# Kernel tuning notes

Hardware: AMD Instinct MI355X
Metric: run time of the kernel (lower is better)

## Reference

```python
import jax, jax.numpy as jnp
import numpy as np

N, E, R = 50000, 800000, 3
IN_DIM, HID, HEADS = 128, 128, 4
C = HID // HEADS  # per-head channels = 32
NEG_SLOPE = 0.2   # GATConv default LeakyReLU slope
LN_EPS = 1e-5


def setup_inputs() -> dict:
    key = jax.random.key(0)
    ks = jax.random.split(key, 8)
    x = jax.random.normal(ks[0], (N, IN_DIM), jnp.float32)
    edge_index = jax.random.randint(ks[1], (R, 2, E), 0, N, jnp.int32)
    edge_attr = jax.random.uniform(ks[2], (R, E, 1), dtype=jnp.float32)  # unused by GATConv (edge_dim=None)
    W = jax.random.normal(ks[3], (R, IN_DIM, HID), jnp.float32) / np.float32(np.sqrt(IN_DIM))
    att_src = jax.random.normal(ks[4], (R, HEADS, C), jnp.float32) / np.float32(np.sqrt(C))
    att_dst = jax.random.normal(ks[5], (R, HEADS, C), jnp.float32) / np.float32(np.sqrt(C))
    bias = jnp.zeros((R, HID), jnp.float32)
    gate = jnp.ones((R,), jnp.float32)
    ln_gamma = jnp.ones((HID,), jnp.float32)
    ln_beta = jnp.zeros((HID,), jnp.float32)
    return dict(x=x, edge_index=edge_index, edge_attr=edge_attr, W=W,
                att_src=att_src, att_dst=att_dst, bias=bias, gate=gate,
                ln_gamma=ln_gamma, ln_beta=ln_beta)


def _gat(x, W, a_src, a_dst, b, ei):
    # One GATConv (concat heads, no self loops, eval-mode so no attn dropout).
    h = (x @ W).reshape(N, HEADS, C)                      # [N,H,C]
    alpha_src = jnp.einsum('nhc,hc->nh', h, a_src)        # [N,H]
    alpha_dst = jnp.einsum('nhc,hc->nh', h, a_dst)        # [N,H]
    src, dst = ei[0], ei[1]
    e = jax.nn.leaky_relu(alpha_src[src] + alpha_dst[dst], NEG_SLOPE)  # [E,H]
    # segment-softmax over incoming edges of each dst node
    e_max = jax.ops.segment_max(e, dst, num_segments=N)   # [N,H] (-inf for isolated nodes, never indexed)
    e_exp = jnp.exp(e - e_max[dst])                       # [E,H]
    denom = jax.ops.segment_sum(e_exp, dst, num_segments=N)
    alpha = e_exp / (denom[dst] + 1e-16)                  # [E,H]
    msg = h[src] * alpha[:, :, None]                      # [E,H,C] edge gather + weight
    out = jax.ops.segment_sum(msg, dst, num_segments=N)   # [N,H,C] scatter-aggregate
    return out.reshape(N, HID) + b


def reference(x, edge_index, edge_attr, W, att_src, att_dst, bias, gate, ln_gamma, ln_beta):
    # edge_attr is accepted but unused: GATConv was built without edge_dim.
    outs = jax.vmap(_gat, in_axes=(None, 0, 0, 0, 0, 0))(x, W, att_src, att_dst, bias, edge_index)  # [R,N,HID]
    gw = jax.nn.softmax(gate)                             # gated fusion weights [R]
    h = jnp.einsum('r,rnd->nd', gw, outs)                 # [N,HID]
    h = h + x                                             # rescale = Identity (in_dim == hid)
    mu = jnp.mean(h, axis=-1, keepdims=True)
    var = jnp.var(h, axis=-1, keepdims=True)
    h = (h - mu) / jnp.sqrt(var + LN_EPS) * ln_gamma + ln_beta
    return h, gw  # dropout is identity in eval mode
```

## Files before the change

kernel.cpp:

```cpp
#include <hip/hip_runtime.h>

#define N_NODES 50000
#define E_EDGES 800000
#define R_REL 3
#define HID 128
#define HEADS 4
#define CAP 64
#define NPART 32
#define PSIZE 1563
#define CHUNKS_A 98
#define CAP_A 448

typedef __attribute__((ext_vector_type(8))) short short8;
typedef __attribute__((ext_vector_type(4))) float float4v;

__device__ __forceinline__ unsigned short f2bf(float f) {
    unsigned int u = __float_as_uint(f);
    u += 0x7fffu + ((u >> 16) & 1u);
    return (unsigned short)(u >> 16);
}
__device__ __forceinline__ float bf_lo(unsigned int u) { return __uint_as_float(u << 16); }
__device__ __forceinline__ float bf_hi(unsigned int u) { return __uint_as_float(u & 0xffff0000u); }

#define WCONV_T (R_REL * HID * HID)
#define SETUP_BLKS 193
#define FILLA_BLKS (R_REL * CHUNKS_A)
__global__ __launch_bounds__(256) void setup_fillA_kernel(const float* __restrict__ W,
                                                          const float* __restrict__ gate,
                                                          const int* __restrict__ edge_idx,
                                                          unsigned short* __restrict__ wtb,
                                                          float* __restrict__ gw_out,
                                                          unsigned* __restrict__ regions,
                                                          int* __restrict__ bc) {
    __shared__ unsigned buf[NPART * CAP_A];
    __shared__ int lcnt[NPART];
    int bid = blockIdx.x;
    if (bid < SETUP_BLKS) {
        int tid = bid * 256 + threadIdx.x;
        if (tid < WCONV_T) {
            int r = tid >> 14, rem = tid & 16383, n = rem >> 7, k = rem & 127;
            wtb[tid] = f2bf(W[r * 16384 + k * 128 + n]);
        } else if (tid == WCONV_T) {
            float g0 = gate[0], g1 = gate[1], g2 = gate[2];
            float mg = fmaxf(g0, fmaxf(g1, g2));
            float e0 = __expf(g0 - mg), e1 = __expf(g1 - mg), e2 = __expf(g2 - mg);
            float inv = 1.f / (e0 + e1 + e2);
            gw_out[0] = e0 * inv; gw_out[1] = e1 * inv; gw_out[2] = e2 * inv;
        }
        return;
    }
    int fb = bid - SETUP_BLKS;
    int r = fb / CHUNKS_A, c = fb % CHUNKS_A;
    if (threadIdx.x < NPART) lcnt[threadIdx.x] = 0;
    __syncthreads();
    const int4* s4 = (const int4*)(edge_idx + (long)r * 2 * E_EDGES);
    const int4* d4 = (const int4*)(edge_idx + (long)r * 2 * E_EDGES + E_EDGES);
    int i0 = c * 2048;
    int i1 = i0 + 2048; if (i1 > E_EDGES / 4) i1 = E_EDGES / 4;
    for (int i = i0 + threadIdx.x; i < i1; i += 256) {
        int4 sv = s4[i];
        int4 dv = d4[i];
#pragma unroll
        for (int j = 0; j < 4; ++j) {
            int dst = (j == 0) ? dv.x : (j == 1) ? dv.y : (j == 2) ? dv.z : dv.w;
            int src = (j == 0) ? sv.x : (j == 1) ? sv.y : (j == 2) ? sv.z : sv.w;
            int p = dst / PSIZE;
            int reldst = dst - p * PSIZE;
            int pos = atomicAdd(&lcnt[p], 1);
            if (pos < CAP_A) buf[p * CAP_A + pos] = ((unsigned)reldst << 16) | (unsigned)src;
        }
    }
    __syncthreads();
    long rbase = (long)(r * CHUNKS_A + c) * NPART;
#pragma unroll 4
    for (int p = 0; p < NPART; ++p) {
        int n = lcnt[p]; if (n > CAP_A) n = CAP_A;
        unsigned* dp = regions + (rbase + p) * CAP_A;
        for (int i = threadIdx.x; i < n; i += 256) dp[i] = buf[p * CAP_A + i];
    }
    if (threadIdx.x < NPART) {
        int n = lcnt[threadIdx.x]; if (n > CAP_A) n = CAP_A;
        bc[rbase + threadIdx.x] = n;
    }
}

#define FILLB_BLKS (R_REL * NPART)
#define STRIPS 3125
#define BLK_PER_REL 782
#define GEMM_BLKS (R_REL * BLK_PER_REL)
__global__ __launch_bounds__(256) void gemm_fillB_kernel(const float* __restrict__ x,
                                                         const unsigned short* __restrict__ wtb,
                                                         unsigned short* __restrict__ hb,
                                                         const float* __restrict__ att_src,
                                                         const float* __restrict__ att_dst,
                                                         float* __restrict__ asrc,
                                                         float* __restrict__ adst,
                                                         const unsigned* __restrict__ regions,
                                                         const int* __restrict__ bc,
                                                         int* __restrict__ cnt,
                                                         unsigned short* __restrict__ slots) {
    __shared__ int lc[PSIZE];
    int bid = blockIdx.x;
    if (bid < FILLB_BLKS) {
        int r = bid / NPART, p = bid % NPART;
        int base = p * PSIZE;
        int psz = N_NODES - base; if (psz > PSIZE) psz = PSIZE;
        for (int i = threadIdx.x; i < PSIZE; i += 256) lc[i] = 0;
        __syncthreads();
        for (int c = 0; c < CHUNKS_A; ++c) {
            long rb = (long)(r * CHUNKS_A + c) * NPART + p;
            int n = bc[rb];
            const unsigned* sp = regions + rb * CAP_A;
            for (int i = threadIdx.x; i < n; i += 256) {
                unsigned e = sp[i];
                int reldst = e >> 16;
                int src = e & 0xffff;
                int pos = atomicAdd(&lc[reldst], 1);
                if (pos < CAP)
                    slots[((long)(r * N_NODES + base + reldst)) * CAP + pos] = (unsigned short)src;
            }
        }
        __syncthreads();
        for (int i = threadIdx.x; i < psz; i += 256)
            cnt[r * N_NODES + base + i] = lc[i];
        return;
    }
    int gb = bid - FILLB_BLKS;
    int r = gb / BLK_PER_REL;
    int sb = gb % BLK_PER_REL;
    int strip = sb * 4 + (threadIdx.x >> 6);
    if (strip >= STRIPS) return;
    int lane = threadIdx.x & 63;
    int m = lane & 15, quad = lane >> 4;

    const float* xrow = x + (long)(strip * 16 + m) * HID + quad * 8;
    short8 B[4];
#pragma unroll
    for (int kc = 0; kc < 4; ++kc) {
        float4 f0 = *(const float4*)(xrow + kc * 32);
        float4 f1 = *(const float4*)(xrow + kc * 32 + 4);
        short8 b;
        b[0] = (short)f2bf(f0.x); b[1] = (short)f2bf(f0.y);
        b[2] = (short)f2bf(f0.z); b[3] = (short)f2bf(f0.w);
        b[4] = (short)f2bf(f1.x); b[5] = (short)f2bf(f1.y);
        b[6] = (short)f2bf(f1.z); b[7] = (short)f2bf(f1.w);
        B[kc] = b;
    }

    const unsigned short* wt = wtb + r * HID * HID;
    float4v acc[8];
#pragma unroll
    for (int cb = 0; cb < 8; ++cb) acc[cb] = (float4v){0.f, 0.f, 0.f, 0.f};
#pragma unroll
    for (int cb = 0; cb < 8; ++cb) {
        const unsigned short* wrow = wt + (cb * 16 + m) * HID + quad * 8;
#pragma unroll
        for (int kc = 0; kc < 4; ++kc) {
            short8 A = *(const short8*)(wrow + kc * 32);
            acc[cb] = __builtin_amdgcn_mfma_f32_16x16x32_bf16(A, B[kc], acc[cb], 0, 0, 0);
        }
    }
    int node = strip * 16 + m;
    unsigned short* hrow = hb + ((long)r * N_NODES + node) * HID;
#pragma unroll
    for (int cb = 0; cb < 8; ++cb) {
        uint2 o;
        o.x = f2bf(acc[cb][0]) | ((unsigned)f2bf(acc[cb][1]) << 16);
        o.y = f2bf(acc[cb][2]) | ((unsigned)f2bf(acc[cb][3]) << 16);
        *(uint2*)(hrow + cb * 16 + quad * 4) = o;
    }
    const float* ar = att_src + r * HID;
    const float* dr = att_dst + r * HID;
    float sa[4] = {0.f, 0.f, 0.f, 0.f}, sd[4] = {0.f, 0.f, 0.f, 0.f};
#pragma unroll
    for (int cb = 0; cb < 8; ++cb) {
        int hd = cb >> 1;
#pragma unroll
        for (int i = 0; i < 4; ++i) {
            int c = cb * 16 + quad * 4 + i;
            sa[hd] += acc[cb][i] * ar[c];
            sd[hd] += acc[cb][i] * dr[c];
        }
    }
#pragma unroll
    for (int hd = 0; hd < 4; ++hd) {
        sa[hd] += __shfl_xor(sa[hd], 16, 64); sa[hd] += __shfl_xor(sa[hd], 32, 64);
        sd[hd] += __shfl_xor(sd[hd], 16, 64); sd[hd] += __shfl_xor(sd[hd], 32, 64);
    }
    float wa = quad == 0 ? sa[0] : quad == 1 ? sa[1] : quad == 2 ? sa[2] : sa[3];
    float wd = quad == 0 ? sd[0] : quad == 1 ? sd[1] : quad == 2 ? sd[2] : sd[3];
    asrc[((long)r * N_NODES + node) * 4 + quad] = wa;
    adst[((long)r * N_NODES + node) * 4 + quad] = wd;
}

__global__ __launch_bounds__(256) void aggr_kernel(const unsigned short* __restrict__ hb,
                                                   const int* __restrict__ cnt,
                                                   const unsigned short* __restrict__ slots,
                                                   const float* __restrict__ asrc,
                                                   const float* __restrict__ adst,
                                                   const float* __restrict__ gate,
                                                   const float* __restrict__ x,
                                                   const float* __restrict__ bias,
                                                   const float* __restrict__ ln_g,
                                                   const float* __restrict__ ln_b,
                                                   float* __restrict__ out) {
    int node = blockIdx.x * 4 + (threadIdx.x >> 6);
    int lane = threadIdx.x & 63;
    int q = lane >> 4;
    int l = lane & 15;
    int hd = l >> 2;
    float g0 = gate[0], g1 = gate[1], g2 = gate[2];
    float mg = fmaxf(g0, fmaxf(g1, g2));
    float e0 = __expf(g0 - mg), e1 = __expf(g1 - mg), e2 = __expf(g2 - mg);
    float ginv = 1.f / (e0 + e1 + e2);
    float gwv[R_REL] = {e0 * ginv, e1 * ginv, e2 * ginv};

    float run0 = 0.f, run1 = 0.f, run2 = 0.f, run3 = 0.f;
    float run4 = 0.f, run5 = 0.f, run6 = 0.f, run7 = 0.f;
#pragma unroll
    for (int r = 0; r < R_REL; ++r) {
        const unsigned short* hr = hb + (long)r * N_NODES * HID;
        const float* as = asrc + (long)r * N_NODES * 4;
        const float* ad = adst + (long)r * N_NODES * 4;
        int cb = r * N_NODES + node;
        int deg = cnt[cb]; deg = deg < CAP ? deg : CAP;
        const unsigned short* sl = slots + (long)cb * CAP;
        float adv = ad[node * 4 + hd];
        float a0 = 0.f, a1 = 0.f, a2 = 0.f, a3 = 0.f;
        float a4 = 0.f, a5 = 0.f, a6 = 0.f, a7 = 0.f, den = 0.f;
        int i = q;
        for (; i + 12 < deg; i += 16) {
            int s0i = sl[i], s1i = sl[i + 4], s2i = sl[i + 8], s3i = sl[i + 12];
            uint4 u0 = ((const uint4*)(hr + (long)s0i * HID))[l];
            uint4 u1 = ((const uint4*)(hr + (long)s1i * HID))[l];
            uint4 u2 = ((const uint4*)(hr + (long)s2i * HID))[l];
            uint4 u3 = ((const uint4*)(hr + (long)s3i * HID))[l];
            float t0 = as[s0i * 4 + hd] + adv; t0 = t0 > 0.f ? t0 : 0.2f * t0;
            float t1 = as[s1i * 4 + hd] + adv; t1 = t1 > 0.f ? t1 : 0.2f * t1;
            float t2 = as[s2i * 4 + hd] + adv; t2 = t2 > 0.f ? t2 : 0.2f * t2;
            float t3 = as[s3i * 4 + hd] + adv; t3 = t3 > 0.f ? t3 : 0.2f * t3;
            float ev0 = __expf(t0), ev1 = __expf(t1), ev2 = __expf(t2), ev3 = __expf(t3);
            a0 += ev0 * bf_lo(u0.x); a1 += ev0 * bf_hi(u0.x);
            a2 += ev0 * bf_lo(u0.y); a3 += ev0 * bf_hi(u0.y);
            a4 += ev0 * bf_lo(u0.z); a5 += ev0 * bf_hi(u0.z);
            a6 += ev0 * bf_lo(u0.w); a7 += ev0 * bf_hi(u0.w);
            a0 += ev1 * bf_lo(u1.x); a1 += ev1 * bf_hi(u1.x);
            a2 += ev1 * bf_lo(u1.y); a3 += ev1 * bf_hi(u1.y);
            a4 += ev1 * bf_lo(u1.z); a5 += ev1 * bf_hi(u1.z);
            a6 += ev1 * bf_lo(u1.w); a7 += ev1 * bf_hi(u1.w);
            a0 += ev2 * bf_lo(u2.x); a1 += ev2 * bf_hi(u2.x);
            a2 += ev2 * bf_lo(u2.y); a3 += ev2 * bf_hi(u2.y);
            a4 += ev2 * bf_lo(u2.z); a5 += ev2 * bf_hi(u2.z);
            a6 += ev2 * bf_lo(u2.w); a7 += ev2 * bf_hi(u2.w);
            a0 += ev3 * bf_lo(u3.x); a1 += ev3 * bf_hi(u3.x);
            a2 += ev3 * bf_lo(u3.y); a3 += ev3 * bf_hi(u3.y);
            a4 += ev3 * bf_lo(u3.z); a5 += ev3 * bf_hi(u3.z);
            a6 += ev3 * bf_lo(u3.w); a7 += ev3 * bf_hi(u3.w);
            den += (ev0 + ev1) + (ev2 + ev3);
        }
        for (; i < deg; i += 4) {
            int src = sl[i];
            uint4 u = ((const uint4*)(hr + (long)src * HID))[l];
            float s = as[src * 4 + hd] + adv;
            s = s > 0.f ? s : 0.2f * s;
            float ev = __expf(s);
            a0 += ev * bf_lo(u.x); a1 += ev * bf_hi(u.x);
            a2 += ev * bf_lo(u.y); a3 += ev * bf_hi(u.y);
            a4 += ev * bf_lo(u.z); a5 += ev * bf_hi(u.z);
            a6 += ev * bf_lo(u.w); a7 += ev * bf_hi(u.w);
            den += ev;
        }
        a0 += __shfl_xor(a0, 16, 64); a0 += __shfl_xor(a0, 32, 64);
        a1 += __shfl_xor(a1, 16, 64); a1 += __shfl_xor(a1, 32, 64);
        a2 += __shfl_xor(a2, 16, 64); a2 += __shfl_xor(a2, 32, 64);
        a3 += __shfl_xor(a3, 16, 64); a3 += __shfl_xor(a3, 32, 64);
        a4 += __shfl_xor(a4, 16, 64); a4 += __shfl_xor(a4, 32, 64);
        a5 += __shfl_xor(a5, 16, 64); a5 += __shfl_xor(a5, 32, 64);
        a6 += __shfl_xor(a6, 16, 64); a6 += __shfl_xor(a6, 32, 64);
        a7 += __shfl_xor(a7, 16, 64); a7 += __shfl_xor(a7, 32, 64);
        den += __shfl_xor(den, 16, 64); den += __shfl_xor(den, 32, 64);
        float inv = gwv[r] / (den + 1e-16f);
        run0 += a0 * inv; run1 += a1 * inv; run2 += a2 * inv; run3 += a3 * inv;
        run4 += a4 * inv; run5 += a5 * inv; run6 += a6 * inv; run7 += a7 * inv;
    }
    const float4* b4 = (const float4*)bias;
    float4 b00 = b4[2 * l], b01 = b4[2 * l + 1];
    float4 b10 = b4[32 + 2 * l], b11 = b4[32 + 2 * l + 1];
    float4 b20 = b4[64 + 2 * l], b21 = b4[64 + 2 * l + 1];
    float4 xv0 = ((const float4*)x)[(long)node * 32 + 2 * l];
    float4 xv1 = ((const float4*)x)[(long)node * 32 + 2 * l + 1];
    float v0 = run0 + xv0.x + gwv[0] * b00.x + gwv[1] * b10.x + gwv[2] * b20.x;
    float v1 = run1 + xv0.y + gwv[0] * b00.y + gwv[1] * b10.y + gwv[2] * b20.y;
    float v2 = run2 + xv0.z + gwv[0] * b00.z + gwv[1] * b10.z + gwv[2] * b20.z;
    float v3 = run3 + xv0.w + gwv[0] * b00.w + gwv[1] * b10.w + gwv[2] * b20.w;
    float v4 = run4 + xv1.x + gwv[0] * b01.x + gwv[1] * b11.x + gwv[2] * b21.x;
    float v5 = run5 + xv1.y + gwv[0] * b01.y + gwv[1] * b11.y + gwv[2] * b21.y;
    float v6 = run6 + xv1.z + gwv[0] * b01.z + gwv[1] * b11.z + gwv[2] * b21.z;
    float v7 = run7 + xv1.w + gwv[0] * b01.w + gwv[1] * b11.w + gwv[2] * b21.w;
    float sum = v0 + v1 + v2 + v3 + v4 + v5 + v6 + v7;
    float sq = v0 * v0 + v1 * v1 + v2 * v2 + v3 * v3 + v4 * v4 + v5 * v5 + v6 * v6 + v7 * v7;
#pragma unroll
    for (int off = 32; off > 0; off >>= 1) {
        sum += __shfl_xor(sum, off, 64);
        sq  += __shfl_xor(sq, off, 64);
    }
    float mean = sum * (1.f / (4 * HID));
    float var = sq * (1.f / (4 * HID)) - mean * mean;
    float rstd = rsqrtf(var + 1e-5f);
    if (q == 0) {
        float4 gv0 = ((const float4*)ln_g)[2 * l], gv1 = ((const float4*)ln_g)[2 * l + 1];
        float4 bv0 = ((const float4*)ln_b)[2 * l], bv1 = ((const float4*)ln_b)[2 * l + 1];
        float4 o0, o1;
        o0.x = (v0 - mean) * rstd * gv0.x + bv0.x;
        o0.y = (v1 - mean) * rstd * gv0.y + bv0.y;
        o0.z = (v2 - mean) * rstd * gv0.z + bv0.z;
        o0.w = (v3 - mean) * rstd * gv0.w + bv0.w;
        o1.x = (v4 - mean) * rstd * gv1.x + bv1.x;
        o1.y = (v5 - mean) * rstd * gv1.y + bv1.y;
        o1.z = (v6 - mean) * rstd * gv1.z + bv1.z;
        o1.w = (v7 - mean) * rstd * gv1.w + bv1.w;
        ((float4*)out)[(long)node * 32 + 2 * l] = o0;
        ((float4*)out)[(long)node * 32 + 2 * l + 1] = o1;
    }
}

extern "C" void kernel_launch(void* const* d_in, const int* in_sizes, int n_in,
                              void* d_out, int out_size, void* d_ws, size_t ws_size,
                              hipStream_t stream) {
    const float* x        = (const float*)d_in[0];
    const int*   edge_idx = (const int*)d_in[1];
    const float* W        = (const float*)d_in[3];
    const float* att_src  = (const float*)d_in[4];
    const float* att_dst  = (const float*)d_in[5];
    const float* bias     = (const float*)d_in[6];
    const float* gate     = (const float*)d_in[7];
    const float* ln_g     = (const float*)d_in[8];
    const float* ln_b     = (const float*)d_in[9];
    float* out = (float*)d_out;

    unsigned short* hb  = (unsigned short*)d_ws;
    float* asrc = (float*)(hb + (long)R_REL * N_NODES * HID);
    float* adst = asrc + R_REL * N_NODES * HEADS;
    int*   cnt  = (int*)(adst + R_REL * N_NODES * HEADS);
    unsigned short* wtb = (unsigned short*)(cnt + R_REL * N_NODES);
    unsigned short* slots = wtb + R_REL * HID * HID;
    unsigned* regions = (unsigned*)(slots + (long)R_REL * N_NODES * CAP);
    int* bc = (int*)(regions + (long)R_REL * CHUNKS_A * NPART * CAP_A);

    setup_fillA_kernel<<<SETUP_BLKS + FILLA_BLKS, 256, 0, stream>>>(
        W, gate, edge_idx, wtb, out + (long)N_NODES * HID, regions, bc);
    gemm_fillB_kernel<<<FILLB_BLKS + GEMM_BLKS, 256, 0, stream>>>(
        x, wtb, hb, att_src, att_dst, asrc, adst, regions, bc, cnt, slots);
    aggr_kernel<<<N_NODES / 4, 256, 0, stream>>>(hb, cnt, slots, asrc, adst, gate,
                                                 x, bias, ln_g, ln_b, out);
}
```

Measured before the change: 365.9 us.

## Replace two-pass partitioned edge bucketing with direct global-atomic scatter

```diff
diff --git a/kernel.cpp b/kernel.cpp
--- a/kernel.cpp
+++ b/kernel.cpp
@@ -6,10 +6,6 @@
 #define HID 128
 #define HEADS 4
 #define CAP 64
-#define NPART 32
-#define PSIZE 1563
-#define CHUNKS_A 98
-#define CAP_A 448
 
 typedef __attribute__((ext_vector_type(8))) short short8;
 typedef __attribute__((ext_vector_type(4))) float float4v;
@@ -24,16 +20,16 @@
 
 #define WCONV_T (R_REL * HID * HID)
 #define SETUP_BLKS 193
-#define FILLA_BLKS (R_REL * CHUNKS_A)
-__global__ __launch_bounds__(256) void setup_fillA_kernel(const float* __restrict__ W,
-                                                          const float* __restrict__ gate,
-                                                          const int* __restrict__ edge_idx,
-                                                          unsigned short* __restrict__ wtb,
-                                                          float* __restrict__ gw_out,
-                                                          unsigned* __restrict__ regions,
-                                                          int* __restrict__ bc) {
-    __shared__ unsigned buf[NPART * CAP_A];
-    __shared__ int lcnt[NPART];
+#define SCAT_CHUNK 2048
+#define SCAT_PER_REL ((E_EDGES + SCAT_CHUNK - 1) / SCAT_CHUNK)
+#define SCAT_BLKS (R_REL * SCAT_PER_REL)
+__global__ __launch_bounds__(256) void setup_scatter_kernel(const float* __restrict__ W,
+                                                            const float* __restrict__ gate,
+                                                            const int* __restrict__ edge_idx,
+                                                            unsigned short* __restrict__ wtb,
+                                                            float* __restrict__ gw_out,
+                                                            int* __restrict__ cnt,
+                                                            unsigned short* __restrict__ slots) {
     int bid = blockIdx.x;
     if (bid < SETUP_BLKS) {
         int tid = bid * 256 + threadIdx.x;
@@ -50,82 +46,40 @@
         return;
     }
     int fb = bid - SETUP_BLKS;
-    int r = fb / CHUNKS_A, c = fb % CHUNKS_A;
-    if (threadIdx.x < NPART) lcnt[threadIdx.x] = 0;
-    __syncthreads();
+    int r = fb / SCAT_PER_REL, c = fb % SCAT_PER_REL;
     const int4* s4 = (const int4*)(edge_idx + (long)r * 2 * E_EDGES);
     const int4* d4 = (const int4*)(edge_idx + (long)r * 2 * E_EDGES + E_EDGES);
-    int i0 = c * 2048;
-    int i1 = i0 + 2048; if (i1 > E_EDGES / 4) i1 = E_EDGES / 4;
-    for (int i = i0 + threadIdx.x; i < i1; i += 256) {
-        int4 sv = s4[i];
-        int4 dv = d4[i];
-#pragma unroll
-        for (int j = 0; j < 4; ++j) {
-            int dst = (j == 0) ? dv.x : (j == 1) ? dv.y : (j == 2) ? dv.z : dv.w;
-            int src = (j == 0) ? sv.x : (j == 1) ? sv.y : (j == 2) ? sv.z : sv.w;
-            int p = dst / PSIZE;
-            int reldst = dst - p * PSIZE;
-            int pos = atomicAdd(&lcnt[p], 1);
-            if (pos < CAP_A) buf[p * CAP_A + pos] = ((unsigned)reldst << 16) | (unsigned)src;
-        }
-    }
-    __syncthreads();
-    long rbase = (long)(r * CHUNKS_A + c) * NPART;
-#pragma unroll 4
-    for (int p = 0; p < NPART; ++p) {
-        int n = lcnt[p]; if (n > CAP_A) n = CAP_A;
-        unsigned* dp = regions + (rbase + p) * CAP_A;
-        for (int i = threadIdx.x; i < n; i += 256) dp[i] = buf[p * CAP_A + i];
-    }
-    if (threadIdx.x < NPART) {
-        int n = lcnt[threadIdx.x]; if (n > CAP_A) n = CAP_A;
-        bc[rbase + threadIdx.x] = n;
-    }
-}
-
-#define FILLB_BLKS (R_REL * NPART)
+    int* cr = cnt + r * N_NODES;
+    unsigned short* sr = slots + (long)r * N_NODES * CAP;
+    int base4 = c * (SCAT_CHUNK / 4);
+#pragma unroll
+    for (int k = 0; k < 2; ++k) {
+        int i = base4 + k * 256 + threadIdx.x;
+        if (i < E_EDGES / 4) {
+            int4 sv = s4[i];
+            int4 dv = d4[i];
+#pragma unroll
+            for (int j = 0; j < 4; ++j) {
+                int dst = (j == 0) ? dv.x : (j == 1) ? dv.y : (j == 2) ? dv.z : dv.w;
+                int src = (j == 0) ? sv.x : (j == 1) ? sv.y : (j == 2) ? sv.z : sv.w;
+                int p_ = atomicAdd(&cr[dst], 1);
+                if (p_ < CAP) sr[(long)dst * CAP + p_] = (unsigned short)src;
+            }
+        }
+    }
+}
+
 #define STRIPS 3125
 #define BLK_PER_REL 782
 #define GEMM_BLKS (R_REL * BLK_PER_REL)
-__global__ __launch_bounds__(256) void gemm_fillB_kernel(const float* __restrict__ x,
-                                                         const unsigned short* __restrict__ wtb,
-                                                         unsigned short* __restrict__ hb,
-                                                         const float* __restrict__ att_src,
-                                                         const float* __restrict__ att_dst,
-                                                         float* __restrict__ asrc,
-                                                         float* __restrict__ adst,
-                                                         const unsigned* __restrict__ regions,
-                                                         const int* __restrict__ bc,
-                                                         int* __restrict__ cnt,
-                                                         unsigned short* __restrict__ slots) {
-    __shared__ int lc[PSIZE];
-    int bid = blockIdx.x;
-    if (bid < FILLB_BLKS) {
-        int r = bid / NPART, p = bid % NPART;
-        int base = p * PSIZE;
-        int psz = N_NODES - base; if (psz > PSIZE) psz = PSIZE;
-        for (int i = threadIdx.x; i < PSIZE; i += 256) lc[i] = 0;
-        __syncthreads();
-        for (int c = 0; c < CHUNKS_A; ++c) {
-            long rb = (long)(r * CHUNKS_A + c) * NPART + p;
-            int n = bc[rb];
-            const unsigned* sp = regions + rb * CAP_A;
-            for (int i = threadIdx.x; i < n; i += 256) {
-                unsigned e = sp[i];
-                int reldst = e >> 16;
-                int src = e & 0xffff;
-                int pos = atomicAdd(&lc[reldst], 1);
-                if (pos < CAP)
-                    slots[((long)(r * N_NODES + base + reldst)) * CAP + pos] = (unsigned short)src;
-            }
-        }
-        __syncthreads();
-        for (int i = threadIdx.x; i < psz; i += 256)
-            cnt[r * N_NODES + base + i] = lc[i];
-        return;
-    }
-    int gb = bid - FILLB_BLKS;
+__global__ __launch_bounds__(256) void gemm_kernel(const float* __restrict__ x,
+                                                   const unsigned short* __restrict__ wtb,
+                                                   unsigned short* __restrict__ hb,
+                                                   const float* __restrict__ att_src,
+                                                   const float* __restrict__ att_dst,
+                                                   float* __restrict__ asrc,
+                                                   float* __restrict__ adst) {
+    int gb = blockIdx.x;
     int r = gb / BLK_PER_REL;
     int sb = gb % BLK_PER_REL;
     int strip = sb * 4 + (threadIdx.x >> 6);
@@ -228,9 +182,13 @@
         float adv = ad[node * 4 + hd];
         float a0 = 0.f, a1 = 0.f, a2 = 0.f, a3 = 0.f;
         float a4 = 0.f, a5 = 0.f, a6 = 0.f, a7 = 0.f, den = 0.f;
-        int i = q;
-        for (; i + 12 < deg; i += 16) {
-            int s0i = sl[i], s1i = sl[i + 4], s2i = sl[i + 8], s3i = sl[i + 12];
+        for (int i = q; i < deg; i += 16) {
+            int j1 = i + 4, j2 = i + 8, j3 = i + 12;
+            bool v1 = j1 < deg, v2 = j2 < deg, v3 = j3 < deg;
+            int s0i = sl[i];
+            int s1i = sl[v1 ? j1 : i];
+            int s2i = sl[v2 ? j2 : i];
+            int s3i = sl[v3 ? j3 : i];
             uint4 u0 = ((const uint4*)(hr + (long)s0i * HID))[l];
             uint4 u1 = ((const uint4*)(hr + (long)s1i * HID))[l];
             uint4 u2 = ((const uint4*)(hr + (long)s2i * HID))[l];
@@ -239,7 +197,10 @@
             float t1 = as[s1i * 4 + hd] + adv; t1 = t1 > 0.f ? t1 : 0.2f * t1;
             float t2 = as[s2i * 4 + hd] + adv; t2 = t2 > 0.f ? t2 : 0.2f * t2;
             float t3 = as[s3i * 4 + hd] + adv; t3 = t3 > 0.f ? t3 : 0.2f * t3;
-            float ev0 = __expf(t0), ev1 = __expf(t1), ev2 = __expf(t2), ev3 = __expf(t3);
+            float ev0 = __expf(t0);
+            float ev1 = v1 ? __expf(t1) : 0.f;
+            float ev2 = v2 ? __expf(t2) : 0.f;
+            float ev3 = v3 ? __expf(t3) : 0.f;
             a0 += ev0 * bf_lo(u0.x); a1 += ev0 * bf_hi(u0.x);
             a2 += ev0 * bf_lo(u0.y); a3 += ev0 * bf_hi(u0.y);
             a4 += ev0 * bf_lo(u0.z); a5 += ev0 * bf_hi(u0.z);
@@ -258,18 +219,6 @@
             a6 += ev3 * bf_lo(u3.w); a7 += ev3 * bf_hi(u3.w);
             den += (ev0 + ev1) + (ev2 + ev3);
         }
-        for (; i < deg; i += 4) {
-            int src = sl[i];
-            uint4 u = ((const uint4*)(hr + (long)src * HID))[l];
-            float s = as[src * 4 + hd] + adv;
-            s = s > 0.f ? s : 0.2f * s;
-            float ev = __expf(s);
-            a0 += ev * bf_lo(u.x); a1 += ev * bf_hi(u.x);
-            a2 += ev * bf_lo(u.y); a3 += ev * bf_hi(u.y);
-            a4 += ev * bf_lo(u.z); a5 += ev * bf_hi(u.z);
-            a6 += ev * bf_lo(u.w); a7 += ev * bf_hi(u.w);
-            den += ev;
-        }
         a0 += __shfl_xor(a0, 16, 64); a0 += __shfl_xor(a0, 32, 64);
         a1 += __shfl_xor(a1, 16, 64); a1 += __shfl_xor(a1, 32, 64);
         a2 += __shfl_xor(a2, 16, 64); a2 += __shfl_xor(a2, 32, 64);
@@ -344,13 +293,11 @@
     int*   cnt  = (int*)(adst + R_REL * N_NODES * HEADS);
     unsigned short* wtb = (unsigned short*)(cnt + R_REL * N_NODES);
     unsigned short* slots = wtb + R_REL * HID * HID;
-    unsigned* regions = (unsigned*)(slots + (long)R_REL * N_NODES * CAP);
-    int* bc = (int*)(regions + (long)R_REL * CHUNKS_A * NPART * CAP_A);
-
-    setup_fillA_kernel<<<SETUP_BLKS + FILLA_BLKS, 256, 0, stream>>>(
-        W, gate, edge_idx, wtb, out + (long)N_NODES * HID, regions, bc);
-    gemm_fillB_kernel<<<FILLB_BLKS + GEMM_BLKS, 256, 0, stream>>>(
-        x, wtb, hb, att_src, att_dst, asrc, adst, regions, bc, cnt, slots);
+
+    hipMemsetAsync(cnt, 0, (size_t)R_REL * N_NODES * sizeof(int), stream);
+    setup_scatter_kernel<<<SETUP_BLKS + SCAT_BLKS, 256, 0, stream>>>(
+        W, gate, edge_idx, wtb, out + (long)N_NODES * HID, cnt, slots);
+    gemm_kernel<<<GEMM_BLKS, 256, 0, stream>>>(x, wtb, hb, att_src, att_dst, asrc, adst);
     aggr_kernel<<<N_NODES / 4, 256, 0, stream>>>(hb, cnt, slots, asrc, adst, gate,
                                                  x, bias, ln_g, ln_b, out);
 }
```

Measured after the change: 467.9 us. 27.9% more time.

## Double partitions, warp-split region copy/fill, and vectorize slot loads in aggregation

Applied to the files above, without the earlier changes.

```diff
diff --git a/kernel.cpp b/kernel.cpp
--- a/kernel.cpp
+++ b/kernel.cpp
@@ -6,10 +6,10 @@
 #define HID 128
 #define HEADS 4
 #define CAP 64
-#define NPART 32
-#define PSIZE 1563
+#define NPART 64
+#define PSIZE 782
 #define CHUNKS_A 98
-#define CAP_A 448
+#define CAP_A 224
 
 typedef __attribute__((ext_vector_type(8))) short short8;
 typedef __attribute__((ext_vector_type(4))) float float4v;
@@ -72,11 +72,11 @@
     }
     __syncthreads();
     long rbase = (long)(r * CHUNKS_A + c) * NPART;
-#pragma unroll 4
-    for (int p = 0; p < NPART; ++p) {
+    int wv = threadIdx.x >> 6, ln = threadIdx.x & 63;
+    for (int p = wv; p < NPART; p += 4) {
         int n = lcnt[p]; if (n > CAP_A) n = CAP_A;
         unsigned* dp = regions + (rbase + p) * CAP_A;
-        for (int i = threadIdx.x; i < n; i += 256) dp[i] = buf[p * CAP_A + i];
+        for (int i = ln; i < n; i += 64) dp[i] = buf[p * CAP_A + i];
     }
     if (threadIdx.x < NPART) {
         int n = lcnt[threadIdx.x]; if (n > CAP_A) n = CAP_A;
@@ -105,13 +105,15 @@
         int r = bid / NPART, p = bid % NPART;
         int base = p * PSIZE;
         int psz = N_NODES - base; if (psz > PSIZE) psz = PSIZE;
+        if (psz < 0) psz = 0;
         for (int i = threadIdx.x; i < PSIZE; i += 256) lc[i] = 0;
         __syncthreads();
-        for (int c = 0; c < CHUNKS_A; ++c) {
+        int wv = threadIdx.x >> 6, ln = threadIdx.x & 63;
+        for (int c = wv; c < CHUNKS_A; c += 4) {
             long rb = (long)(r * CHUNKS_A + c) * NPART + p;
             int n = bc[rb];
             const unsigned* sp = regions + rb * CAP_A;
-            for (int i = threadIdx.x; i < n; i += 256) {
+            for (int i = ln; i < n; i += 64) {
                 unsigned e = sp[i];
                 int reldst = e >> 16;
                 int src = e & 0xffff;
@@ -225,50 +227,59 @@
         int cb = r * N_NODES + node;
         int deg = cnt[cb]; deg = deg < CAP ? deg : CAP;
         const unsigned short* sl = slots + (long)cb * CAP;
+        const uint2* sl2 = (const uint2*)sl;
         float adv = ad[node * 4 + hd];
         float a0 = 0.f, a1 = 0.f, a2 = 0.f, a3 = 0.f;
         float a4 = 0.f, a5 = 0.f, a6 = 0.f, a7 = 0.f, den = 0.f;
-        int i = q;
-        for (; i + 12 < deg; i += 16) {
-            int s0i = sl[i], s1i = sl[i + 4], s2i = sl[i + 8], s3i = sl[i + 12];
-            uint4 u0 = ((const uint4*)(hr + (long)s0i * HID))[l];
-            uint4 u1 = ((const uint4*)(hr + (long)s1i * HID))[l];
-            uint4 u2 = ((const uint4*)(hr + (long)s2i * HID))[l];
-            uint4 u3 = ((const uint4*)(hr + (long)s3i * HID))[l];
-            float t0 = as[s0i * 4 + hd] + adv; t0 = t0 > 0.f ? t0 : 0.2f * t0;
-            float t1 = as[s1i * 4 + hd] + adv; t1 = t1 > 0.f ? t1 : 0.2f * t1;
-            float t2 = as[s2i * 4 + hd] + adv; t2 = t2 > 0.f ? t2 : 0.2f * t2;
-            float t3 = as[s3i * 4 + hd] + adv; t3 = t3 > 0.f ? t3 : 0.2f * t3;
-            float ev0 = __expf(t0), ev1 = __expf(t1), ev2 = __expf(t2), ev3 = __expf(t3);
-            a0 += ev0 * bf_lo(u0.x); a1 += ev0 * bf_hi(u0.x);
-            a2 += ev0 * bf_lo(u0.y); a3 += ev0 * bf_hi(u0.y);
-            a4 += ev0 * bf_lo(u0.z); a5 += ev0 * bf_hi(u0.z);
-            a6 += ev0 * bf_lo(u0.w); a7 += ev0 * bf_hi(u0.w);
-            a0 += ev1 * bf_lo(u1.x); a1 += ev1 * bf_hi(u1.x);
-            a2 += ev1 * bf_lo(u1.y); a3 += ev1 * bf_hi(u1.y);
-            a4 += ev1 * bf_lo(u1.z); a5 += ev1 * bf_hi(u1.z);
-            a6 += ev1 * bf_lo(u1.w); a7 += ev1 * bf_hi(u1.w);
-            a0 += ev2 * bf_lo(u2.x); a1 += ev2 * bf_hi(u2.x);
-            a2 += ev2 * bf_lo(u2.y); a3 += ev2 * bf_hi(u2.y);
-            a4 += ev2 * bf_lo(u2.z); a5 += ev2 * bf_hi(u2.z);
-            a6 += ev2 * bf_lo(u2.w); a7 += ev2 * bf_hi(u2.w);
-            a0 += ev3 * bf_lo(u3.x); a1 += ev3 * bf_hi(u3.x);
-            a2 += ev3 * bf_lo(u3.y); a3 += ev3 * bf_hi(u3.y);
-            a4 += ev3 * bf_lo(u3.z); a5 += ev3 * bf_hi(u3.z);
-            a6 += ev3 * bf_lo(u3.w); a7 += ev3 * bf_hi(u3.w);
-            den += (ev0 + ev1) + (ev2 + ev3);
-        }
-        for (; i < deg; i += 4) {
-            int src = sl[i];
-            uint4 u = ((const uint4*)(hr + (long)src * HID))[l];
-            float s = as[src * 4 + hd] + adv;
-            s = s > 0.f ? s : 0.2f * s;
-            float ev = __expf(s);
-            a0 += ev * bf_lo(u.x); a1 += ev * bf_hi(u.x);
-            a2 += ev * bf_lo(u.y); a3 += ev * bf_hi(u.y);
-            a4 += ev * bf_lo(u.z); a5 += ev * bf_hi(u.z);
-            a6 += ev * bf_lo(u.w); a7 += ev * bf_hi(u.w);
-            den += ev;
+        if (deg > 0) {
+            int sfb = sl[0];
+            uint2 P0 = sl2[q];
+            uint2 P1 = sl2[q + 4];
+            uint2 P2 = sl2[q + 8];
+            uint2 P3 = sl2[q + 12];
+#define AGGR_ROUND(P, BASE)                                                          \
+            {                                                                        \
+                int b = (BASE) + 4 * q;                                              \
+                int s0 = (int)((P).x & 0xffffu), s1 = (int)((P).x >> 16);            \
+                int s2 = (int)((P).y & 0xffffu), s3 = (int)((P).y >> 16);            \
+                bool v0 = b < deg, v1 = b + 1 < deg, v2 = b + 2 < deg, v3 = b + 3 < deg; \
+                s0 = v0 ? s0 : sfb; s1 = v1 ? s1 : sfb;                              \
+                s2 = v2 ? s2 : sfb; s3 = v3 ? s3 : sfb;                              \
+                uint4 u0 = ((const uint4*)(hr + (long)s0 * HID))[l];                 \
+                uint4 u1 = ((const uint4*)(hr + (long)s1 * HID))[l];                 \
+                uint4 u2 = ((const uint4*)(hr + (long)s2 * HID))[l];                 \
+                uint4 u3 = ((const uint4*)(hr + (long)s3 * HID))[l];                 \
+                float t0 = as[s0 * 4 + hd] + adv; t0 = t0 > 0.f ? t0 : 0.2f * t0;    \
+                float t1 = as[s1 * 4 + hd] + adv; t1 = t1 > 0.f ? t1 : 0.2f * t1;    \
+                float t2 = as[s2 * 4 + hd] + adv; t2 = t2 > 0.f ? t2 : 0.2f * t2;    \
+                float t3 = as[s3 * 4 + hd] + adv; t3 = t3 > 0.f ? t3 : 0.2f * t3;    \
+                float ev0 = v0 ? __expf(t0) : 0.f;                                   \
+                float ev1 = v1 ? __expf(t1) : 0.f;                                   \
+                float ev2 = v2 ? __expf(t2) : 0.f;                                   \
+                float ev3 = v3 ? __expf(t3) : 0.f;                                   \
+                a0 += ev0 * bf_lo(u0.x); a1 += ev0 * bf_hi(u0.x);                    \
+                a2 += ev0 * bf_lo(u0.y); a3 += ev0 * bf_hi(u0.y);                    \
+                a4 += ev0 * bf_lo(u0.z); a5 += ev0 * bf_hi(u0.z);                    \
+                a6 += ev0 * bf_lo(u0.w); a7 += ev0 * bf_hi(u0.w);                    \
+                a0 += ev1 * bf_lo(u1.x); a1 += ev1 * bf_hi(u1.x);                    \
+                a2 += ev1 * bf_lo(u1.y); a3 += ev1 * bf_hi(u1.y);                    \
+                a4 += ev1 * bf_lo(u1.z); a5 += ev1 * bf_hi(u1.z);                    \
+                a6 += ev1 * bf_lo(u1.w); a7 += ev1 * bf_hi(u1.w);                    \
+                a0 += ev2 * bf_lo(u2.x); a1 += ev2 * bf_hi(u2.x);                    \
+                a2 += ev2 * bf_lo(u2.y); a3 += ev2 * bf_hi(u2.y);                    \
+                a4 += ev2 * bf_lo(u2.z); a5 += ev2 * bf_hi(u2.z);                    \
+                a6 += ev2 * bf_lo(u2.w); a7 += ev2 * bf_hi(u2.w);                    \
+                a0 += ev3 * bf_lo(u3.x); a1 += ev3 * bf_hi(u3.x);                    \
+                a2 += ev3 * bf_lo(u3.y); a3 += ev3 * bf_hi(u3.y);                    \
+                a4 += ev3 * bf_lo(u3.z); a5 += ev3 * bf_hi(u3.z);                    \
+                a6 += ev3 * bf_lo(u3.w); a7 += ev3 * bf_hi(u3.w);                    \
+                den += (ev0 + ev1) + (ev2 + ev3);                                    \
+            }
+            AGGR_ROUND(P0, 0)
+            if (deg > 16) { AGGR_ROUND(P1, 16) }
+            if (deg > 32) { AGGR_ROUND(P2, 32) }
+            if (deg > 48) { AGGR_ROUND(P3, 48) }
+#undef AGGR_ROUND
         }
         a0 += __shfl_xor(a0, 16, 64); a0 += __shfl_xor(a0, 32, 64);
         a1 += __shfl_xor(a1, 16, 64); a1 += __shfl_xor(a1, 32, 64);
```

Result: faster. 304.9 us (-16.7%).
